# Performance work log

Measured on AMD Instinct MI355X. Metric: run time of the kernel, lower is better.

## Reference

```python
import jax, jax.numpy as jnp
import numpy as np

SEQ = 8192
IN_DIM = 1024
HIDDEN_DIM = 2048
N_EXPERTS = 8
TOPK = 2


def setup_inputs() -> dict:
    key = jax.random.key(0)
    ks = jax.random.split(key, 6)
    scale = 0.02
    inp = jax.random.normal(ks[0], (SEQ, IN_DIM), jnp.float32)
    weights = jax.random.uniform(ks[1], (SEQ, TOPK), jnp.float32)
    selections = jax.random.randint(ks[2], (SEQ, TOPK), 0, N_EXPERTS, jnp.int32)
    up_proj = jax.random.normal(ks[3], (HIDDEN_DIM * N_EXPERTS, IN_DIM), jnp.float32) * scale
    gate_proj = jax.random.normal(ks[4], (HIDDEN_DIM * N_EXPERTS, IN_DIM), jnp.float32) * scale
    down_proj = jax.random.normal(ks[5], (HIDDEN_DIM * N_EXPERTS, IN_DIM), jnp.float32) * scale
    return {"inp": inp, "weights": weights, "up_proj": up_proj,
            "gate_proj": gate_proj, "down_proj": down_proj, "selections": selections}


def reference(inp, weights, up_proj, gate_proj, down_proj, selections):
    seq, in_dim = inp.shape
    topk = selections.shape[-1]
    # dispatch: replicate each token topk times -> (seq*topk, in_dim)
    x = jnp.broadcast_to(inp[:, None, :], (seq, topk, in_dim)).reshape(-1, in_dim)
    e_ids = selections.reshape(-1)  # (seq*topk,) expert id per dispatched token
    W_up = up_proj.reshape(N_EXPERTS, HIDDEN_DIM, in_dim)
    W_gate = gate_proj.reshape(N_EXPERTS, HIDDEN_DIM, in_dim)
    W_down = down_proj.reshape(N_EXPERTS, HIDDEN_DIM, in_dim)
    out = jnp.zeros_like(x)
    # grouped (block-sparse) GEMM: loop over the small fixed expert set,
    # masking tokens not routed to this expert (gelu(0)*0 = 0, so math matches).
    for e in range(N_EXPERTS):
        mask = (e_ids == e)[:, None]
        xe = jnp.where(mask, x, 0.0)
        h = xe @ W_up[e].T        # (seq*topk, hidden)
        g = xe @ W_gate[e].T      # (seq*topk, hidden)
        out = out + jnp.where(mask, (jax.nn.gelu(g) * h) @ W_down[e], 0.0)
    # combine: weighted sum over topk expert outputs per token
    return (out.reshape(seq, topk, in_dim) * weights[:, :, None]).sum(axis=1)
```

## Files before the change

kernel.cpp:

```cpp
#include <hip/hip_runtime.h>


#define SEQ 8192
#define IN_DIM 1024
#define HID 2048
#define NEXP 8
#define TOPK 2
#define NSLOT (SEQ * TOPK)

#define BM 128
#define BK 64
#define MAX_TILES 136

typedef unsigned short ushort_t;
typedef __bf16 bf16x8 __attribute__((ext_vector_type(8)));
typedef float f32x4 __attribute__((ext_vector_type(4)));

__device__ __forceinline__ ushort_t f2bf(float f) {
    union { float f; unsigned u; } v;
    v.f = f;
    unsigned r = v.u + 0x7FFFu + ((v.u >> 16) & 1u);
    return (ushort_t)(r >> 16);
}

__device__ __forceinline__ float gelu_tanh(float x) {
    float u = 0.7978845608028654f * x * (1.0f + 0.044715f * x * x);
    return x / (1.0f + __expf(-2.0f * u));
}

__device__ __forceinline__ void async16(const void* g, void* l) {
    __builtin_amdgcn_global_load_lds(
        (const __attribute__((address_space(1))) unsigned int*)g,
        (__attribute__((address_space(3))) unsigned int*)l, 16, 0, 0);
}

__device__ __forceinline__ void wait8_barrier() {
    asm volatile("s_waitcnt vmcnt(8)\ns_barrier" ::: "memory");
}
__device__ __forceinline__ void wait0_barrier() {
    asm volatile("s_waitcnt vmcnt(0)\ns_barrier" ::: "memory");
}
__device__ __forceinline__ void lds_barrier() {
    asm volatile("s_waitcnt lgkmcnt(0)\ns_barrier" ::: "memory");
}

__global__ void cast_bf16_kernel(const float* __restrict__ in,
                                 ushort_t* __restrict__ out, int n) {
    int i = (blockIdx.x * blockDim.x + threadIdx.x) * 4;
    if (i >= n) return;
    float4 v = *(const float4*)(in + i);
    union { ushort_t u[4]; uint2 v; } o;
    o.u[0] = f2bf(v.x); o.u[1] = f2bf(v.y);
    o.u[2] = f2bf(v.z); o.u[3] = f2bf(v.w);
    *(uint2*)(out + i) = o.v;
}

__global__ void transpose_cast_kernel(const float* __restrict__ in,
                                      ushort_t* __restrict__ out) {
    __shared__ float tile[32][33];
    int e = blockIdx.z;
    int d0 = blockIdx.x * 32, h0 = blockIdx.y * 32;
    int tx = threadIdx.x & 31, ty = threadIdx.x >> 5;
    const float* src = in + (size_t)e * HID * IN_DIM;
    for (int j = 0; j < 32; j += 8)
        tile[ty + j][tx] = src[(size_t)(h0 + ty + j) * IN_DIM + d0 + tx];
    __syncthreads();
    ushort_t* dst = out + (size_t)e * IN_DIM * HID;
    for (int j = 0; j < 32; j += 8)
        dst[(size_t)(d0 + ty + j) * HID + h0 + tx] = f2bf(tile[tx][ty + j]);
}

__global__ void route_kernel(const int* __restrict__ sel,
                             const float* __restrict__ wts,
                             int* __restrict__ meta,
                             int* __restrict__ stok,
                             int* __restrict__ sinv) {
    __shared__ int lc[256][NEXP];
    __shared__ int tot[NEXP];
    __shared__ int s_off[NEXP + 1];
    int t = threadIdx.x;
    int cnt[NEXP];
#pragma unroll
    for (int e = 0; e < NEXP; e++) cnt[e] = 0;
    int base = t * (NSLOT / 256);
    for (int i = 0; i < NSLOT / 256; i++) cnt[sel[base + i]]++;
#pragma unroll
    for (int e = 0; e < NEXP; e++) lc[t][e] = cnt[e];
    __syncthreads();
    if (t < NEXP) {
        int run = 0;
        for (int i = 0; i < 256; i++) { int v = lc[i][t]; lc[i][t] = run; run += v; }
        tot[t] = run;
    }
    __syncthreads();
    if (t == 0) {
        int o = 0;
        for (int e = 0; e < NEXP; e++) { s_off[e] = o; o += tot[e]; }
        s_off[NEXP] = o;
        for (int e = 0; e <= NEXP; e++) meta[e] = s_off[e];
        int nt = 0;
        for (int e = 0; e < NEXP; e++) {
            int c = s_off[e + 1] - s_off[e];
            int m = (c + BM - 1) / BM;
            for (int i = 0; i < m; i++) { meta[32 + 2 * nt] = e; meta[33 + 2 * nt] = i; nt++; }
        }
        meta[16] = nt;
    }
    __syncthreads();
    int cur[NEXP];
#pragma unroll
    for (int e = 0; e < NEXP; e++) cur[e] = s_off[e] + lc[t][e];
    for (int i = 0; i < NSLOT / 256; i++) {
        int slot = base + i;
        int e = sel[slot];
        int pos = cur[e]++;
        stok[pos] = slot >> 1;
        sinv[slot] = pos;
    }
}

__global__ __launch_bounds__(256) void gemm1_kernel(
    const ushort_t* __restrict__ X,
    const ushort_t* __restrict__ U,
    const ushort_t* __restrict__ G,
    const int* __restrict__ meta,
    const int* __restrict__ stok,
    ushort_t* __restrict__ act) {
    __shared__ __align__(16) ushort_t XT[2][BM * BK];
    __shared__ __align__(16) ushort_t UT[2][64 * BK];
    __shared__ __align__(16) ushort_t GT[2][64 * BK];
    __shared__ int s_tok[BM];

    int tile = blockIdx.x;
    if (tile >= meta[16]) return;
    int e = meta[32 + 2 * tile];
    int mt = meta[33 + 2 * tile];
    int off = meta[e];
    int cnt = meta[e + 1] - off;
    int m0 = mt * BM;
    int n0 = blockIdx.y * 64;

    int tid = threadIdx.x;
    if (tid < BM) {
        int r = m0 + tid;
        if (r >= cnt) r = cnt - 1;
        s_tok[tid] = stok[off + r];
    }
    __syncthreads();

    int lane = tid & 63;
    int w = tid >> 6;
    int wr = w >> 1, wc = w & 1;
    int srow = lane >> 3;
    int schunk = lane & 7;
    int gchunk = schunk ^ srow;

    const ushort_t* Ue = U + ((size_t)e * HID + n0) * IN_DIM;
    const ushort_t* Ge = G + ((size_t)e * HID + n0) * IN_DIM;

    const ushort_t* xp[4];
    const ushort_t* up2[2];
    const ushort_t* gp2[2];
#pragma unroll
    for (int i = 0; i < 4; i++) {
        int r = w * 32 + i * 8 + srow;
        xp[i] = X + (size_t)s_tok[r] * IN_DIM + gchunk * 8;
    }
#pragma unroll
    for (int i = 0; i < 2; i++) {
        int r = w * 16 + i * 8 + srow;
        up2[i] = Ue + (size_t)r * IN_DIM + gchunk * 8;
        gp2[i] = Ge + (size_t)r * IN_DIM + gchunk * 8;
    }

    f32x4 accH[4][2], accG[4][2];
#pragma unroll
    for (int mi = 0; mi < 4; mi++)
#pragma unroll
        for (int ni = 0; ni < 2; ni++) {
            accH[mi][ni] = (f32x4){0.f, 0.f, 0.f, 0.f};
            accG[mi][ni] = (f32x4){0.f, 0.f, 0.f, 0.f};
        }

    int r4 = lane & 15;
    int q = lane >> 4;
    int sw7 = r4 & 7;

#define G1_ISSUE(s)                                                        \
    {                                                                      \
        int _b = (s) & 1;                                                  \
        int _k0 = (s) * BK;                                                \
        _Pragma("unroll")                                                  \
        for (int i = 0; i < 4; i++)                                        \
            async16(xp[i] + _k0, &XT[_b][(w * 32 + i * 8) * BK]);          \
        _Pragma("unroll")                                                  \
        for (int i = 0; i < 2; i++) {                                      \
            async16(up2[i] + _k0, &UT[_b][(w * 16 + i * 8) * BK]);         \
            async16(gp2[i] + _k0, &GT[_b][(w * 16 + i * 8) * BK]);         \
        }                                                                  \
    }

#define G1_COMPUTE(s)                                                      \
    {                                                                      \
        int _b = (s) & 1;                                                  \
        _Pragma("unroll")                                                  \
        for (int kk = 0; kk < BK; kk += 32) {                              \
            int c = (kk >> 3) + q;                                         \
            int cs = ((c ^ sw7) << 3);                                     \
            bf16x8 a[4], bu[2], bg[2];                                     \
            _Pragma("unroll")                                              \
            for (int i = 0; i < 4; i++)                                    \
                a[i] = *(const bf16x8*)&XT[_b][(wr * 64 + i * 16 + r4) * BK + cs]; \
            _Pragma("unroll")                                              \
            for (int i = 0; i < 2; i++) {                                  \
                bu[i] = *(const bf16x8*)&UT[_b][(wc * 32 + i * 16 + r4) * BK + cs]; \
                bg[i] = *(const bf16x8*)&GT[_b][(wc * 32 + i * 16 + r4) * BK + cs]; \
            }                                                              \
            _Pragma("unroll")                                              \
            for (int mi = 0; mi < 4; mi++)                                 \
                _Pragma("unroll")                                          \
                for (int ni = 0; ni < 2; ni++) {                           \
                    accH[mi][ni] = __builtin_amdgcn_mfma_f32_16x16x32_bf16(\
                        a[mi], bu[ni], accH[mi][ni], 0, 0, 0);             \
                    accG[mi][ni] = __builtin_amdgcn_mfma_f32_16x16x32_bf16(\
                        a[mi], bg[ni], accG[mi][ni], 0, 0, 0);             \
                }                                                          \
        }                                                                  \
    }

    const int NK = IN_DIM / BK;
    G1_ISSUE(0);
    for (int s = 0; s < NK - 1; s++) {
        G1_ISSUE(s + 1);
        wait8_barrier();
        G1_COMPUTE(s);
        lds_barrier();
    }
    wait0_barrier();
    G1_COMPUTE(NK - 1);

#pragma unroll
    for (int mi = 0; mi < 4; mi++) {
#pragma unroll
        for (int r = 0; r < 4; r++) {
            int row_local = wr * 64 + mi * 16 + q * 4 + r;
            int grow = m0 + row_local;
            if (grow >= cnt) continue;
            size_t orow = (size_t)(off + grow) * HID + n0 + wc * 32;
#pragma unroll
            for (int ni = 0; ni < 2; ni++) {
                float h = accH[mi][ni][r];
                float g = accG[mi][ni][r];
                act[orow + ni * 16 + r4] = f2bf(gelu_tanh(g) * h);
            }
        }
    }
}

__global__ __launch_bounds__(256) void gemm2_kernel(
    const ushort_t* __restrict__ act,
    const ushort_t* __restrict__ DT,
    const int* __restrict__ meta,
    float* __restrict__ y) {
    __shared__ __align__(16) ushort_t AT[2][BM * BK];
    __shared__ __align__(16) ushort_t BT[2][BM * BK];

    int tile = blockIdx.x;
    if (tile >= meta[16]) return;
    int e = meta[32 + 2 * tile];
    int mt = meta[33 + 2 * tile];
    int off = meta[e];
    int cnt = meta[e + 1] - off;
    int m0 = mt * BM;
    int n0 = blockIdx.y * 128;

    int tid = threadIdx.x;
    int lane = tid & 63;
    int w = tid >> 6;
    int wr = w >> 1, wc = w & 1;
    int srow = lane >> 3;
    int schunk = lane & 7;
    int gchunk = schunk ^ srow;

    const ushort_t* Ae = act + (size_t)off * HID;
    const ushort_t* Be = DT + ((size_t)e * IN_DIM + n0) * HID;

    const ushort_t* ap[4];
    const ushort_t* bp[4];
#pragma unroll
    for (int i = 0; i < 4; i++) {
        int r = w * 32 + i * 8 + srow;
        int ar = m0 + r; if (ar >= cnt) ar = cnt - 1;
        ap[i] = Ae + (size_t)ar * HID + gchunk * 8;
        bp[i] = Be + (size_t)r * HID + gchunk * 8;
    }

    f32x4 acc[4][4];
#pragma unroll
    for (int mi = 0; mi < 4; mi++)
#pragma unroll
        for (int ni = 0; ni < 4; ni++) acc[mi][ni] = (f32x4){0.f, 0.f, 0.f, 0.f};

    int r4 = lane & 15;
    int q = lane >> 4;
    int sw7 = r4 & 7;

#define G2_ISSUE(s)                                                        \
    {                                                                      \
        int _b = (s) & 1;                                                  \
        int _k0 = (s) * BK;                                                \
        _Pragma("unroll")                                                  \
        for (int i = 0; i < 4; i++) {                                      \
            async16(ap[i] + _k0, &AT[_b][(w * 32 + i * 8) * BK]);          \
            async16(bp[i] + _k0, &BT[_b][(w * 32 + i * 8) * BK]);          \
        }                                                                  \
    }

#define G2_COMPUTE(s)                                                      \
    {                                                                      \
        int _b = (s) & 1;                                                  \
        _Pragma("unroll")                                                  \
        for (int kk = 0; kk < BK; kk += 32) {                              \
            int c = (kk >> 3) + q;                                         \
            int cs = ((c ^ sw7) << 3);                                     \
            bf16x8 a[4], b[4];                                             \
            _Pragma("unroll")                                              \
            for (int i = 0; i < 4; i++) {                                  \
                a[i] = *(const bf16x8*)&AT[_b][(wr * 64 + i * 16 + r4) * BK + cs]; \
                b[i] = *(const bf16x8*)&BT[_b][(wc * 64 + i * 16 + r4) * BK + cs]; \
            }                                                              \
            _Pragma("unroll")                                              \
            for (int mi = 0; mi < 4; mi++)                                 \
                _Pragma("unroll")                                          \
                for (int ni = 0; ni < 4; ni++)                             \
                    acc[mi][ni] = __builtin_amdgcn_mfma_f32_16x16x32_bf16( \
                        a[mi], b[ni], acc[mi][ni], 0, 0, 0);               \
        }                                                                  \
    }

    const int NK = HID / BK;
    G2_ISSUE(0);
    for (int s = 0; s < NK - 1; s++) {
        G2_ISSUE(s + 1);
        wait8_barrier();
        G2_COMPUTE(s);
        lds_barrier();
    }
    wait0_barrier();
    G2_COMPUTE(NK - 1);

#pragma unroll
    for (int mi = 0; mi < 4; mi++) {
#pragma unroll
        for (int r = 0; r < 4; r++) {
            int row_local = wr * 64 + mi * 16 + q * 4 + r;
            int grow = m0 + row_local;
            if (grow >= cnt) continue;
            float* orow = y + (size_t)(off + grow) * IN_DIM + n0 + wc * 64;
#pragma unroll
            for (int ni = 0; ni < 4; ni++)
                orow[ni * 16 + r4] = acc[mi][ni][r];
        }
    }
}

__global__ __launch_bounds__(256) void combine_kernel(
    const float* __restrict__ y,
    const float* __restrict__ wts,
    const int* __restrict__ sinv,
    float* __restrict__ out) {
    int tok = blockIdx.x;
    int c = threadIdx.x;
    int p0 = sinv[tok * 2], p1 = sinv[tok * 2 + 1];
    float w0 = wts[tok * 2], w1 = wts[tok * 2 + 1];
    float4 a = *(const float4*)(y + (size_t)p0 * IN_DIM + c * 4);
    float4 b = *(const float4*)(y + (size_t)p1 * IN_DIM + c * 4);
    float4 o;
    o.x = w0 * a.x + w1 * b.x;
    o.y = w0 * a.y + w1 * b.y;
    o.z = w0 * a.z + w1 * b.z;
    o.w = w0 * a.w + w1 * b.w;
    *(float4*)(out + (size_t)tok * IN_DIM + c * 4) = o;
}

extern "C" void kernel_launch(void* const* d_in, const int* in_sizes, int n_in,
                              void* d_out, int out_size, void* d_ws, size_t ws_size,
                              hipStream_t stream) {
    const float* inp  = (const float*)d_in[0];
    const float* wts  = (const float*)d_in[1];
    const float* up   = (const float*)d_in[2];
    const float* gate = (const float*)d_in[3];
    const float* down = (const float*)d_in[4];
    const int*   sel  = (const int*)d_in[5];
    float* out = (float*)d_out;

    char* ws = (char*)d_ws;
    ushort_t* inp_bf  = (ushort_t*)(ws);
    ushort_t* up_bf   = (ushort_t*)(ws + 16777216);
    ushort_t* gate_bf = (ushort_t*)(ws + 50331648);
    ushort_t* down_bf = (ushort_t*)(ws + 83886080);
    ushort_t* act     = (ushort_t*)(ws + 117440512);
    int*      stok    = (int*)(ws + 184549376);
    int*      sinv    = (int*)(ws + 184614912);
    int*      meta    = (int*)(ws + 184680448);
    float*    y       = (float*)(ws);

    cast_bf16_kernel<<<(SEQ * IN_DIM) / 1024, 256, 0, stream>>>(inp, inp_bf, SEQ * IN_DIM);
    cast_bf16_kernel<<<(NEXP * HID * IN_DIM) / 1024, 256, 0, stream>>>(up, up_bf, NEXP * HID * IN_DIM);
    cast_bf16_kernel<<<(NEXP * HID * IN_DIM) / 1024, 256, 0, stream>>>(gate, gate_bf, NEXP * HID * IN_DIM);
    transpose_cast_kernel<<<dim3(IN_DIM / 32, HID / 32, NEXP), 256, 0, stream>>>(down, down_bf);
    route_kernel<<<1, 256, 0, stream>>>(sel, wts, meta, stok, sinv);
    gemm1_kernel<<<dim3(MAX_TILES, HID / 64), 256, 0, stream>>>(inp_bf, up_bf, gate_bf, meta, stok, act);
    gemm2_kernel<<<dim3(MAX_TILES, IN_DIM / 128), 256, 0, stream>>>(act, down_bf, meta, y);
    combine_kernel<<<SEQ, 256, 0, stream>>>(y, wts, sinv, out);
}
```

Baseline: 613.3 us.

## Widen gemm1 N tile to 128, halve BK, swap grid axes

Gemm1's N tile grows from 64 to 128 columns, so each block computes 128x128 for both up and gate, doubling accumulators and the reuse of each X tile. BK drops from 64 to 32 in both GEMMs to keep LDS within budget, which needs a new 4-chunk XOR swizzle, precomputed LDS offsets and adjusted vmcnt waits. Grid axes are swapped so N tiles of the same M tile run next to each other, aiming for better L2 reuse of the gathered activations. The cost is higher register pressure (64 accumulator vectors in gemm1) and twice as many barriers per K.

```diff
diff --git a/kernel.cpp b/kernel.cpp
--- a/kernel.cpp
+++ b/kernel.cpp
@@ -9,7 +9,7 @@
 #define NSLOT (SEQ * TOPK)
 
 #define BM 128
-#define BK 64
+#define BK 32
 #define MAX_TILES 136
 
 typedef unsigned short ushort_t;
@@ -34,8 +34,11 @@
         (__attribute__((address_space(3))) unsigned int*)l, 16, 0, 0);
 }
 
-__device__ __forceinline__ void wait8_barrier() {
-    asm volatile("s_waitcnt vmcnt(8)\ns_barrier" ::: "memory");
+__device__ __forceinline__ void wait6_barrier() {
+    asm volatile("s_waitcnt vmcnt(6)\ns_barrier" ::: "memory");
+}
+__device__ __forceinline__ void wait4_barrier() {
+    asm volatile("s_waitcnt vmcnt(4)\ns_barrier" ::: "memory");
 }
 __device__ __forceinline__ void wait0_barrier() {
     asm volatile("s_waitcnt vmcnt(0)\ns_barrier" ::: "memory");
@@ -127,18 +130,18 @@
     const int* __restrict__ stok,
     ushort_t* __restrict__ act) {
     __shared__ __align__(16) ushort_t XT[2][BM * BK];
-    __shared__ __align__(16) ushort_t UT[2][64 * BK];
-    __shared__ __align__(16) ushort_t GT[2][64 * BK];
+    __shared__ __align__(16) ushort_t UT[2][BM * BK];
+    __shared__ __align__(16) ushort_t GT[2][BM * BK];
     __shared__ int s_tok[BM];
 
-    int tile = blockIdx.x;
+    int tile = blockIdx.y;
     if (tile >= meta[16]) return;
     int e = meta[32 + 2 * tile];
     int mt = meta[33 + 2 * tile];
     int off = meta[e];
     int cnt = meta[e + 1] - off;
     int m0 = mt * BM;
-    int n0 = blockIdx.y * 64;
+    int n0 = blockIdx.x * 128;
 
     int tid = threadIdx.x;
     if (tid < BM) {
@@ -151,88 +154,82 @@
     int lane = tid & 63;
     int w = tid >> 6;
     int wr = w >> 1, wc = w & 1;
-    int srow = lane >> 3;
-    int schunk = lane & 7;
-    int gchunk = schunk ^ srow;
+    int srow = lane >> 2;
+    int schunk = lane & 3;
+    int gchunk = schunk ^ ((srow >> 1) & 3);
 
     const ushort_t* Ue = U + ((size_t)e * HID + n0) * IN_DIM;
     const ushort_t* Ge = G + ((size_t)e * HID + n0) * IN_DIM;
 
-    const ushort_t* xp[4];
-    const ushort_t* up2[2];
-    const ushort_t* gp2[2];
-#pragma unroll
-    for (int i = 0; i < 4; i++) {
-        int r = w * 32 + i * 8 + srow;
+    const ushort_t* xp[2];
+    const ushort_t* up[2];
+    const ushort_t* gp[2];
+#pragma unroll
+    for (int i = 0; i < 2; i++) {
+        int r = w * 32 + i * 16 + srow;
         xp[i] = X + (size_t)s_tok[r] * IN_DIM + gchunk * 8;
-    }
-#pragma unroll
-    for (int i = 0; i < 2; i++) {
-        int r = w * 16 + i * 8 + srow;
-        up2[i] = Ue + (size_t)r * IN_DIM + gchunk * 8;
-        gp2[i] = Ge + (size_t)r * IN_DIM + gchunk * 8;
-    }
-
-    f32x4 accH[4][2], accG[4][2];
+        up[i] = Ue + (size_t)r * IN_DIM + gchunk * 8;
+        gp[i] = Ge + (size_t)r * IN_DIM + gchunk * 8;
+    }
+
+    f32x4 accH[4][4], accG[4][4];
 #pragma unroll
     for (int mi = 0; mi < 4; mi++)
 #pragma unroll
-        for (int ni = 0; ni < 2; ni++) {
+        for (int ni = 0; ni < 4; ni++) {
             accH[mi][ni] = (f32x4){0.f, 0.f, 0.f, 0.f};
             accG[mi][ni] = (f32x4){0.f, 0.f, 0.f, 0.f};
         }
 
     int r4 = lane & 15;
     int q = lane >> 4;
-    int sw7 = r4 & 7;
+    int cs = ((q ^ ((r4 >> 1) & 3)) << 3);
+    int xoff[4], noff[4];
+#pragma unroll
+    for (int i = 0; i < 4; i++) {
+        xoff[i] = (wr * 64 + i * 16 + r4) * BK + cs;
+        noff[i] = (wc * 64 + i * 16 + r4) * BK + cs;
+    }
 
 #define G1_ISSUE(s)                                                        \
     {                                                                      \
         int _b = (s) & 1;                                                  \
         int _k0 = (s) * BK;                                                \
         _Pragma("unroll")                                                  \
-        for (int i = 0; i < 4; i++)                                        \
-            async16(xp[i] + _k0, &XT[_b][(w * 32 + i * 8) * BK]);          \
-        _Pragma("unroll")                                                  \
         for (int i = 0; i < 2; i++) {                                      \
-            async16(up2[i] + _k0, &UT[_b][(w * 16 + i * 8) * BK]);         \
-            async16(gp2[i] + _k0, &GT[_b][(w * 16 + i * 8) * BK]);         \
+            int lo = (w * 32 + i * 16) * BK;                               \
+            async16(xp[i] + _k0, &XT[_b][lo]);                             \
+            async16(up[i] + _k0, &UT[_b][lo]);                             \
+            async16(gp[i] + _k0, &GT[_b][lo]);                             \
         }                                                                  \
     }
 
 #define G1_COMPUTE(s)                                                      \
     {                                                                      \
         int _b = (s) & 1;                                                  \
-        _Pragma("unroll")                                                  \
-        for (int kk = 0; kk < BK; kk += 32) {                              \
-            int c = (kk >> 3) + q;                                         \
-            int cs = ((c ^ sw7) << 3);                                     \
-            bf16x8 a[4], bu[2], bg[2];                                     \
+        bf16x8 a[4], bu[4], bg[4];                                         \
+        _Pragma("unroll")                                                  \
+        for (int i = 0; i < 4; i++) {                                      \
+            a[i]  = *(const bf16x8*)&XT[_b][xoff[i]];                      \
+            bu[i] = *(const bf16x8*)&UT[_b][noff[i]];                      \
+            bg[i] = *(const bf16x8*)&GT[_b][noff[i]];                      \
+        }                                                                  \
+        _Pragma("unroll")                                                  \
+        for (int mi = 0; mi < 4; mi++)                                     \
             _Pragma("unroll")                                              \
-            for (int i = 0; i < 4; i++)                                    \
-                a[i] = *(const bf16x8*)&XT[_b][(wr * 64 + i * 16 + r4) * BK + cs]; \
-            _Pragma("unroll")                                              \
-            for (int i = 0; i < 2; i++) {                                  \
-                bu[i] = *(const bf16x8*)&UT[_b][(wc * 32 + i * 16 + r4) * BK + cs]; \
-                bg[i] = *(const bf16x8*)&GT[_b][(wc * 32 + i * 16 + r4) * BK + cs]; \
+            for (int ni = 0; ni < 4; ni++) {                               \
+                accH[mi][ni] = __builtin_amdgcn_mfma_f32_16x16x32_bf16(    \
+                    a[mi], bu[ni], accH[mi][ni], 0, 0, 0);                 \
+                accG[mi][ni] = __builtin_amdgcn_mfma_f32_16x16x32_bf16(    \
+                    a[mi], bg[ni], accG[mi][ni], 0, 0, 0);                 \
             }                                                              \
-            _Pragma("unroll")                                              \
-            for (int mi = 0; mi < 4; mi++)                                 \
-                _Pragma("unroll")                                          \
-                for (int ni = 0; ni < 2; ni++) {                           \
-                    accH[mi][ni] = __builtin_amdgcn_mfma_f32_16x16x32_bf16(\
-                        a[mi], bu[ni], accH[mi][ni], 0, 0, 0);             \
-                    accG[mi][ni] = __builtin_amdgcn_mfma_f32_16x16x32_bf16(\
-                        a[mi], bg[ni], accG[mi][ni], 0, 0, 0);             \
-                }                                                          \
-        }                                                                  \
     }
 
     const int NK = IN_DIM / BK;
     G1_ISSUE(0);
     for (int s = 0; s < NK - 1; s++) {
         G1_ISSUE(s + 1);
-        wait8_barrier();
+        wait6_barrier();
         G1_COMPUTE(s);
         lds_barrier();
     }
@@ -246,9 +243,9 @@
             int row_local = wr * 64 + mi * 16 + q * 4 + r;
             int grow = m0 + row_local;
             if (grow >= cnt) continue;
-            size_t orow = (size_t)(off + grow) * HID + n0 + wc * 32;
-#pragma unroll
-            for (int ni = 0; ni < 2; ni++) {
+            size_t orow = (size_t)(off + grow) * HID + n0 + wc * 64;
+#pragma unroll
+            for (int ni = 0; ni < 4; ni++) {
                 float h = accH[mi][ni][r];
                 float g = accG[mi][ni][r];
                 act[orow + ni * 16 + r4] = f2bf(gelu_tanh(g) * h);
@@ -265,31 +262,31 @@
     __shared__ __align__(16) ushort_t AT[2][BM * BK];
     __shared__ __align__(16) ushort_t BT[2][BM * BK];
 
-    int tile = blockIdx.x;
+    int tile = blockIdx.y;
     if (tile >= meta[16]) return;
     int e = meta[32 + 2 * tile];
     int mt = meta[33 + 2 * tile];
     int off = meta[e];
     int cnt = meta[e + 1] - off;
     int m0 = mt * BM;
-    int n0 = blockIdx.y * 128;
+    int n0 = blockIdx.x * 128;
 
     int tid = threadIdx.x;
     int lane = tid & 63;
     int w = tid >> 6;
     int wr = w >> 1, wc = w & 1;
-    int srow = lane >> 3;
-    int schunk = lane & 7;
-    int gchunk = schunk ^ srow;
+    int srow = lane >> 2;
+    int schunk = lane & 3;
+    int gchunk = schunk ^ ((srow >> 1) & 3);
 
     const ushort_t* Ae = act + (size_t)off * HID;
     const ushort_t* Be = DT + ((size_t)e * IN_DIM + n0) * HID;
 
-    const ushort_t* ap[4];
-    const ushort_t* bp[4];
-#pragma unroll
-    for (int i = 0; i < 4; i++) {
-        int r = w * 32 + i * 8 + srow;
+    const ushort_t* ap[2];
+    const ushort_t* bp[2];
+#pragma unroll
+    for (int i = 0; i < 2; i++) {
+        int r = w * 32 + i * 16 + srow;
         int ar = m0 + r; if (ar >= cnt) ar = cnt - 1;
         ap[i] = Ae + (size_t)ar * HID + gchunk * 8;
         bp[i] = Be + (size_t)r * HID + gchunk * 8;
@@ -303,46 +300,48 @@
 
     int r4 = lane & 15;
     int q = lane >> 4;
-    int sw7 = r4 & 7;
+    int cs = ((q ^ ((r4 >> 1) & 3)) << 3);
+    int aoff[4], boff[4];
+#pragma unroll
+    for (int i = 0; i < 4; i++) {
+        aoff[i] = (wr * 64 + i * 16 + r4) * BK + cs;
+        boff[i] = (wc * 64 + i * 16 + r4) * BK + cs;
+    }
 
 #define G2_ISSUE(s)                                                        \
     {                                                                      \
         int _b = (s) & 1;                                                  \
         int _k0 = (s) * BK;                                                \
         _Pragma("unroll")                                                  \
-        for (int i = 0; i < 4; i++) {                                      \
-            async16(ap[i] + _k0, &AT[_b][(w * 32 + i * 8) * BK]);          \
-            async16(bp[i] + _k0, &BT[_b][(w * 32 + i * 8) * BK]);          \
+        for (int i = 0; i < 2; i++) {                                      \
+            int lo = (w * 32 + i * 16) * BK;                               \
+            async16(ap[i] + _k0, &AT[_b][lo]);                             \
+            async16(bp[i] + _k0, &BT[_b][lo]);                             \
         }                                                                  \
     }
 
 #define G2_COMPUTE(s)                                                      \
     {                                                                      \
         int _b = (s) & 1;                                                  \
-        _Pragma("unroll")                                                  \
-        for (int kk = 0; kk < BK; kk += 32) {                              \
-            int c = (kk >> 3) + q;                                         \
-            int cs = ((c ^ sw7) << 3);                                     \
-            bf16x8 a[4], b[4];                                             \
+        bf16x8 a[4], b[4];                                                 \
+        _Pragma("unroll")                                                  \
+        for (int i = 0; i < 4; i++) {                                      \
+            a[i] = *(const bf16x8*)&AT[_b][aoff[i]];                       \
+            b[i] = *(const bf16x8*)&BT[_b][boff[i]];                       \
+        }                                                                  \
+        _Pragma("unroll")                                                  \
+        for (int mi = 0; mi < 4; mi++)                                     \
             _Pragma("unroll")                                              \
-            for (int i = 0; i < 4; i++) {                                  \
-                a[i] = *(const bf16x8*)&AT[_b][(wr * 64 + i * 16 + r4) * BK + cs]; \
-                b[i] = *(const bf16x8*)&BT[_b][(wc * 64 + i * 16 + r4) * BK + cs]; \
-            }                                                              \
-            _Pragma("unroll")                                              \
-            for (int mi = 0; mi < 4; mi++)                                 \
-                _Pragma("unroll")                                          \
-                for (int ni = 0; ni < 4; ni++)                             \
-                    acc[mi][ni] = __builtin_amdgcn_mfma_f32_16x16x32_bf16( \
-                        a[mi], b[ni], acc[mi][ni], 0, 0, 0);               \
-        }                                                                  \
+            for (int ni = 0; ni < 4; ni++)                                 \
+                acc[mi][ni] = __builtin_amdgcn_mfma_f32_16x16x32_bf16(     \
+                    a[mi], b[ni], acc[mi][ni], 0, 0, 0);                   \
     }
 
     const int NK = HID / BK;
     G2_ISSUE(0);
     for (int s = 0; s < NK - 1; s++) {
         G2_ISSUE(s + 1);
-        wait8_barrier();
+        wait4_barrier();
         G2_COMPUTE(s);
         lds_barrier();
     }
@@ -410,7 +409,7 @@
     cast_bf16_kernel<<<(NEXP * HID * IN_DIM) / 1024, 256, 0, stream>>>(gate, gate_bf, NEXP * HID * IN_DIM);
     transpose_cast_kernel<<<dim3(IN_DIM / 32, HID / 32, NEXP), 256, 0, stream>>>(down, down_bf);
     route_kernel<<<1, 256, 0, stream>>>(sel, wts, meta, stok, sinv);
-    gemm1_kernel<<<dim3(MAX_TILES, HID / 64), 256, 0, stream>>>(inp_bf, up_bf, gate_bf, meta, stok, act);
-    gemm2_kernel<<<dim3(MAX_TILES, IN_DIM / 128), 256, 0, stream>>>(act, down_bf, meta, y);
+    gemm1_kernel<<<dim3(HID / 128, MAX_TILES), 256, 0, stream>>>(inp_bf, up_bf, gate_bf, meta, stok, act);
+    gemm2_kernel<<<dim3(IN_DIM / 128, MAX_TILES), 256, 0, stream>>>(act, down_bf, meta, y);
     combine_kernel<<<SEQ, 256, 0, stream>>>(y, wts, sinv, out);
 }
```

After: 630.9 us. +2.9%, slower.
